# Kernel optimization log

Measured on AMD Instinct MI355X. Metric: run time of the kernel, lower is better.

Reference implementation:

```python
import jax, jax.numpy as jnp
import numpy as np

NUM_SCOPES, NUM_DECOMPS, BATCH, NODES_IN, NUM_SUMS = 128, 8, 1024, 32, 32


def logmatmul(a, b):
    """Stable log-domain matmul: out[..., b, j] = logsumexp_k(a[..., b, k] + b[..., k, j]).
    a: [s, d, B, K], b: [s, d, K, J] -> [s, d, B, J]."""
    max_a = jnp.max(a, axis=-1, keepdims=True)            # [s, d, B, 1]
    max_b = jnp.max(b, axis=-2, keepdims=True)            # [s, d, 1, J]
    prod = jnp.einsum('sdbk,sdkj->sdbj', jnp.exp(a - max_a), jnp.exp(b - max_b))
    return jnp.log(prod) + max_a + max_b


def setup_inputs() -> dict:
    key = jax.random.key(0)
    k1, k2 = jax.random.split(key)
    x = jax.random.normal(k1, (NUM_SCOPES, NUM_DECOMPS, BATCH, NODES_IN), dtype=jnp.float32)
    # accumulators are linear-space (logspace_accumulators=False) and must be > 0
    accumulators = jax.random.uniform(
        k2, (NUM_SCOPES, NUM_DECOMPS, NODES_IN, NUM_SUMS),
        minval=0.1, maxval=1.0, dtype=jnp.float32)
    return {"x": x, "accumulators": accumulators}


def reference(x, accumulators):
    # log_softmax over the nodes_in axis (axis=2) of log(accumulators)
    log_weights = jax.nn.log_softmax(jnp.log(accumulators), axis=2)
    return logmatmul(x, log_weights)  # [s, d, B, num_sums]
```

## Files before the change

kernel.cpp:

```cpp
#include <hip/hip_runtime.h>
#include <stdint.h>


#define THREADS 256
#define ROWS    256
#define EPITCH  40
#define WPITCH  40

typedef __attribute__((ext_vector_type(8))) short short8;
typedef __attribute__((ext_vector_type(4))) float f32x4;

__device__ __forceinline__ uint32_t pack2_bf16(float lo, float hi) {
    uint32_t ul = __builtin_bit_cast(uint32_t, lo);
    uint32_t uh = __builtin_bit_cast(uint32_t, hi);
    ul = (ul + 0x7fffu + ((ul >> 16) & 1u)) >> 16;
    uh = (uh + 0x7fffu + ((uh >> 16) & 1u)) >> 16;
    return ul | (uh << 16);
}

__global__ __launch_bounds__(THREADS, 4) void sws_kernel(
    const float* __restrict__ x,
    const float* __restrict__ acc,
    float* __restrict__ out)
{
    __shared__ float w_f32[32 * 32];
    __shared__ float inv_lds[32];
    __shared__ float m_lds[ROWS];
    __shared__ __align__(16) unsigned short e_lds[ROWS * EPITCH];
    __shared__ __align__(16) unsigned short wt_lds[32 * WPITCH];

    const int t    = threadIdx.x;
    const int blk  = blockIdx.x;
    const int sd   = blk >> 2;
    const int lane = t & 63;
    const int wv   = t >> 6;
    const int l15  = lane & 15;
    const int quad = lane >> 4;

    const float4* x4 = (const float4*)(x + (size_t)blk * ROWS * 32);
    float4 xv[8];
#pragma unroll
    for (int i = 0; i < 8; ++i) xv[i] = x4[t + i * THREADS];

    const float* a_base = acc + (size_t)sd * (32 * 32);
    {
        float av[4];
#pragma unroll
        for (int i = 0; i < 4; ++i) av[i] = a_base[t + i * THREADS];
#pragma unroll
        for (int i = 0; i < 4; ++i) w_f32[t + i * THREADS] = av[i];
    }
    __syncthreads();
    if (t < 32) {
        float s = 0.f;
#pragma unroll
        for (int k = 0; k < 32; ++k) s += w_f32[k * 32 + t];
        inv_lds[t] = 1.0f / s;
    }
    __syncthreads();
#pragma unroll
    for (int i = 0; i < 4; ++i) {
        int idx = t + i * THREADS;
        int k = idx >> 5, j = idx & 31;
        float v = w_f32[idx] * inv_lds[j];
        uint32_t u = __builtin_bit_cast(uint32_t, v);
        u = (u + 0x7fffu + ((u >> 16) & 1u)) >> 16;
        wt_lds[j * WPITCH + k] = (unsigned short)u;
    }

#pragma unroll
    for (int i = 0; i < 8; ++i) {
        float4 v = xv[i];
        float m = fmaxf(fmaxf(v.x, v.y), fmaxf(v.z, v.w));
        m = fmaxf(m, __shfl_xor(m, 1, 64));
        m = fmaxf(m, __shfl_xor(m, 2, 64));
        m = fmaxf(m, __shfl_xor(m, 4, 64));
        int f = t + i * THREADS;
        int row = f >> 3, c4 = f & 7;
        uint32_t p0 = pack2_bf16(__expf(v.x - m), __expf(v.y - m));
        uint32_t p1 = pack2_bf16(__expf(v.z - m), __expf(v.w - m));
        *(uint2*)&e_lds[row * EPITCH + c4 * 4] = make_uint2(p0, p1);
        if (c4 == 0) m_lds[row] = m;
    }
    __syncthreads();

    short8 bfrag[2];
#pragma unroll
    for (int jt = 0; jt < 2; ++jt)
        bfrag[jt] = *(const short8*)&wt_lds[(jt * 16 + l15) * WPITCH + quad * 8];

    f32x4 cacc[4][2];
#pragma unroll
    for (int rt4 = 0; rt4 < 4; ++rt4) {
        int rt = wv * 4 + rt4;
        short8 afrag = *(const short8*)&e_lds[(rt * 16 + l15) * EPITCH + quad * 8];
#pragma unroll
        for (int jt = 0; jt < 2; ++jt)
            cacc[rt4][jt] = __builtin_amdgcn_mfma_f32_16x16x32_bf16(
                afrag, bfrag[jt], (f32x4){0.f, 0.f, 0.f, 0.f}, 0, 0, 0);
    }

    float* obase = out + (size_t)blk * ROWS * 32;
#pragma unroll
    for (int rt4 = 0; rt4 < 4; ++rt4) {
        int rt = wv * 4 + rt4;
        int r0 = rt * 16 + quad * 4;
        float4 mv = *(const float4*)&m_lds[r0];
        float mr[4] = {mv.x, mv.y, mv.z, mv.w};
#pragma unroll
        for (int jt = 0; jt < 2; ++jt) {
            int col = jt * 16 + l15;
#pragma unroll
            for (int r = 0; r < 4; ++r) {
                float val = __logf(cacc[rt4][jt][r]) + mr[r];
                obase[(size_t)(r0 + r) * 32 + col] = val;
            }
        }
    }
}

extern "C" void kernel_launch(void* const* d_in, const int* in_sizes, int n_in,
                              void* d_out, int out_size, void* d_ws, size_t ws_size,
                              hipStream_t stream) {
    const float* x   = (const float*)d_in[0];
    const float* acc = (const float*)d_in[1];
    float* out = (float*)d_out;

    dim3 grid(4096);
    dim3 block(THREADS);
    hipLaunchKernelGGL(sws_kernel, grid, block, 0, stream, x, acc, out);
}
```

Before: 235.6 us.

## Load x directly into MFMA fragments and halve rows per block

Each thread now loads its x values straight in the MFMA A-fragment layout. It computes the row max with cross-quad shuffles and packs exp values into the fragment in registers, so the exp tile and row maxima no longer go through LDS. Row maxima for the epilogue are fetched with a shuffle instead of from shared memory. Blocks now cover 128 rows instead of 256, with the grid doubled and launch bounds raised for higher occupancy. The cost is recomputing the weight normalization in twice as many blocks.

Measured after the change: 231.0 us. About the same (-1.9%).

```diff
diff --git a/kernel.cpp b/kernel.cpp
--- a/kernel.cpp
+++ b/kernel.cpp
@@ -3,12 +3,11 @@
 
 
 #define THREADS 256
-#define ROWS    256
-#define EPITCH  40
-#define WPITCH  40
+#define ROWS    128
 
 typedef __attribute__((ext_vector_type(8))) short short8;
 typedef __attribute__((ext_vector_type(4))) float f32x4;
+typedef __attribute__((ext_vector_type(4))) int   i32x4;
 
 __device__ __forceinline__ uint32_t pack2_bf16(float lo, float hi) {
     uint32_t ul = __builtin_bit_cast(uint32_t, lo);
@@ -18,38 +17,39 @@
     return ul | (uh << 16);
 }
 
-__global__ __launch_bounds__(THREADS, 4) void sws_kernel(
+__device__ __forceinline__ unsigned short bf16_1(float v) {
+    uint32_t u = __builtin_bit_cast(uint32_t, v);
+    return (unsigned short)((u + 0x7fffu + ((u >> 16) & 1u)) >> 16);
+}
+
+__global__ __launch_bounds__(THREADS, 8) void sws_kernel(
     const float* __restrict__ x,
     const float* __restrict__ acc,
     float* __restrict__ out)
 {
     __shared__ float w_f32[32 * 32];
     __shared__ float inv_lds[32];
-    __shared__ float m_lds[ROWS];
-    __shared__ __align__(16) unsigned short e_lds[ROWS * EPITCH];
-    __shared__ __align__(16) unsigned short wt_lds[32 * WPITCH];
+    __shared__ __align__(16) unsigned short wt_lds[32 * 32];
 
     const int t    = threadIdx.x;
     const int blk  = blockIdx.x;
-    const int sd   = blk >> 2;
+    const int sd   = blk >> 3;
     const int lane = t & 63;
     const int wv   = t >> 6;
     const int l15  = lane & 15;
     const int quad = lane >> 4;
 
     const float4* x4 = (const float4*)(x + (size_t)blk * ROWS * 32);
-    float4 xv[8];
+    float4 xv[4];
 #pragma unroll
-    for (int i = 0; i < 8; ++i) xv[i] = x4[t + i * THREADS];
+    for (int i = 0; i < 2; ++i) {
+        int f4 = ((wv * 2 + i) * 16 + l15) * 8 + quad * 2;
+        xv[2 * i]     = x4[f4];
+        xv[2 * i + 1] = x4[f4 + 1];
+    }
 
-    const float* a_base = acc + (size_t)sd * (32 * 32);
-    {
-        float av[4];
-#pragma unroll
-        for (int i = 0; i < 4; ++i) av[i] = a_base[t + i * THREADS];
-#pragma unroll
-        for (int i = 0; i < 4; ++i) w_f32[t + i * THREADS] = av[i];
-    }
+    const float4 a4 = ((const float4*)(acc + (size_t)sd * 1024))[t];
+    *((float4*)&w_f32[t * 4]) = a4;
     __syncthreads();
     if (t < 32) {
         float s = 0.f;
@@ -58,63 +58,57 @@
         inv_lds[t] = 1.0f / s;
     }
     __syncthreads();
-#pragma unroll
-    for (int i = 0; i < 4; ++i) {
-        int idx = t + i * THREADS;
-        int k = idx >> 5, j = idx & 31;
-        float v = w_f32[idx] * inv_lds[j];
-        uint32_t u = __builtin_bit_cast(uint32_t, v);
-        u = (u + 0x7fffu + ((u >> 16) & 1u)) >> 16;
-        wt_lds[j * WPITCH + k] = (unsigned short)u;
+    {
+        const int k = t >> 3, j0 = (t & 7) * 4;
+        const float4 inv4 = *((const float4*)&inv_lds[j0]);
+        wt_lds[(j0 + 0) * 32 + k] = bf16_1(a4.x * inv4.x);
+        wt_lds[(j0 + 1) * 32 + k] = bf16_1(a4.y * inv4.y);
+        wt_lds[(j0 + 2) * 32 + k] = bf16_1(a4.z * inv4.z);
+        wt_lds[(j0 + 3) * 32 + k] = bf16_1(a4.w * inv4.w);
     }
 
+    float  mrow[2];
+    short8 afrag[2];
 #pragma unroll
-    for (int i = 0; i < 8; ++i) {
-        float4 v = xv[i];
-        float m = fmaxf(fmaxf(v.x, v.y), fmaxf(v.z, v.w));
-        m = fmaxf(m, __shfl_xor(m, 1, 64));
-        m = fmaxf(m, __shfl_xor(m, 2, 64));
-        m = fmaxf(m, __shfl_xor(m, 4, 64));
-        int f = t + i * THREADS;
-        int row = f >> 3, c4 = f & 7;
-        uint32_t p0 = pack2_bf16(__expf(v.x - m), __expf(v.y - m));
-        uint32_t p1 = pack2_bf16(__expf(v.z - m), __expf(v.w - m));
-        *(uint2*)&e_lds[row * EPITCH + c4 * 4] = make_uint2(p0, p1);
-        if (c4 == 0) m_lds[row] = m;
+    for (int i = 0; i < 2; ++i) {
+        float4 a = xv[2 * i], b = xv[2 * i + 1];
+        float m = fmaxf(fmaxf(fmaxf(a.x, a.y), fmaxf(a.z, a.w)),
+                        fmaxf(fmaxf(b.x, b.y), fmaxf(b.z, b.w)));
+        m = fmaxf(m, __shfl_xor(m, 16, 64));
+        m = fmaxf(m, __shfl_xor(m, 32, 64));
+        mrow[i] = m;
+        i32x4 pk;
+        pk[0] = (int)pack2_bf16(__expf(a.x - m), __expf(a.y - m));
+        pk[1] = (int)pack2_bf16(__expf(a.z - m), __expf(a.w - m));
+        pk[2] = (int)pack2_bf16(__expf(b.x - m), __expf(b.y - m));
+        pk[3] = (int)pack2_bf16(__expf(b.z - m), __expf(b.w - m));
+        afrag[i] = __builtin_bit_cast(short8, pk);
     }
     __syncthreads();
 
     short8 bfrag[2];
 #pragma unroll
     for (int jt = 0; jt < 2; ++jt)
-        bfrag[jt] = *(const short8*)&wt_lds[(jt * 16 + l15) * WPITCH + quad * 8];
+        bfrag[jt] = *(const short8*)&wt_lds[(jt * 16 + l15) * 32 + quad * 8];
 
-    f32x4 cacc[4][2];
+    f32x4 cacc[2][2];
 #pragma unroll
-    for (int rt4 = 0; rt4 < 4; ++rt4) {
-        int rt = wv * 4 + rt4;
-        short8 afrag = *(const short8*)&e_lds[(rt * 16 + l15) * EPITCH + quad * 8];
+    for (int i = 0; i < 2; ++i)
 #pragma unroll
         for (int jt = 0; jt < 2; ++jt)
-            cacc[rt4][jt] = __builtin_amdgcn_mfma_f32_16x16x32_bf16(
-                afrag, bfrag[jt], (f32x4){0.f, 0.f, 0.f, 0.f}, 0, 0, 0);
-    }
+            cacc[i][jt] = __builtin_amdgcn_mfma_f32_16x16x32_bf16(
+                afrag[i], bfrag[jt], (f32x4){0.f, 0.f, 0.f, 0.f}, 0, 0, 0);
 
-    float* obase = out + (size_t)blk * ROWS * 32;
+    float* ob = out + (size_t)blk * ROWS * 32;
 #pragma unroll
-    for (int rt4 = 0; rt4 < 4; ++rt4) {
-        int rt = wv * 4 + rt4;
-        int r0 = rt * 16 + quad * 4;
-        float4 mv = *(const float4*)&m_lds[r0];
-        float mr[4] = {mv.x, mv.y, mv.z, mv.w};
+    for (int i = 0; i < 2; ++i) {
+        int rbase = ((wv * 2 + i) * 16) + quad * 4;
 #pragma unroll
-        for (int jt = 0; jt < 2; ++jt) {
-            int col = jt * 16 + l15;
-#pragma unroll
-            for (int r = 0; r < 4; ++r) {
-                float val = __logf(cacc[rt4][jt][r]) + mr[r];
-                obase[(size_t)(r0 + r) * 32 + col] = val;
-            }
+        for (int r = 0; r < 4; ++r) {
+            float mr = __shfl(mrow[i], quad * 4 + r, 16);
+            float* orow = ob + (size_t)(rbase + r) * 32;
+            orow[l15]      = __logf(cacc[i][0][r]) + mr;
+            orow[l15 + 16] = __logf(cacc[i][1][r]) + mr;
         }
     }
 }
@@ -126,7 +120,7 @@
     const float* acc = (const float*)d_in[1];
     float* out = (float*)d_out;
 
-    dim3 grid(4096);
+    dim3 grid(8192);
     dim3 block(THREADS);
     hipLaunchKernelGGL(sws_kernel, grid, block, 0, stream, x, acc, out);
 }
```
